# Kernel optimization log

Hardware: AMD Instinct MI355X
Metric: run time of the kernel (lower is better)

The kernel has to match this reference:

```python
import jax, jax.numpy as jnp
import numpy as np


def setup_inputs() -> dict:
    key = jax.random.key(0)
    k1, k2 = jax.random.split(key)
    B, Q, K, H = 8, 2048, 2048, 128
    out_state = jax.random.normal(k1, (B, Q, H), dtype=jnp.float32)
    history = jax.random.normal(k2, (B, K, H), dtype=jnp.float32)
    return {"out_state": out_state, "history": history}


def reference(out_state, history):
    # tanh pre-activation on queries
    q = jnp.tanh(out_state)                              # [B, Q, H]
    # unscaled QK^T scores
    scores = jnp.einsum("bqh,bkh->bqk", q, history)      # [B, Q, K]
    probs = jax.nn.softmax(scores, axis=2)               # softmax over keys
    attn = jnp.einsum("bqk,bkh->bqh", probs, history)    # [B, Q, H]
    return attn
```

## Files before the change

### kernel.cpp

```cpp
#include <hip/hip_runtime.h>
#include <math.h>


typedef _Float16 half8 __attribute__((ext_vector_type(8)));
typedef _Float16 half4 __attribute__((ext_vector_type(4)));
typedef float    f32x4 __attribute__((ext_vector_type(4)));

#define QQ 2048
#define KK 2048
#define HH 128
#define BM 64
#define BN 64
#define NTILES 32
#define KS_STR 136
#define VT_STR 72
#define PS_STR 72
#define L2E 1.44269504f
#define SPLITS_TARGET 3
#define WS_O_FLOATS   ((size_t)256 * BM * HH)
#define WS_ML_FLOATS  ((size_t)256 * BM)

union U32H { unsigned int u; _Float16 h[2]; };

__launch_bounds__(256, 3)
__global__ void attn_main(const float* __restrict__ out_state,
                          const float* __restrict__ history,
                          float* __restrict__ out,
                          float* __restrict__ ws,
                          int splits) {
    __shared__ _Float16 Ks[BN * KS_STR];
    __shared__ _Float16 Vt[HH * VT_STR];
    __shared__ _Float16 Ps[4][16 * PS_STR];

    const int tid  = threadIdx.x;
    const int wave = tid >> 6;
    const int lane = tid & 63;
    const int quad = lane >> 4;
    const int lc   = lane & 15;

    const int bid  = blockIdx.x;
    const int s    = bid >> 8;
    const int r256 = bid & 255;
    const int b    = r256 >> 5;
    const int qb   = r256 & 31;
    const int m0   = qb * BM;

    const int kt0 = (NTILES * s) / splits;
    const int kt1 = (NTILES * (s + 1)) / splits;

    half8 qf[4];
    {
        const int m = m0 + wave * 16 + lc;
        const float* qrow = out_state + ((size_t)b * QQ + m) * HH;
        #pragma unroll
        for (int s4 = 0; s4 < 4; ++s4) {
            const int h0 = 32 * s4 + quad * 8;
            const float4 a = *(const float4*)(qrow + h0);
            const float4 c = *(const float4*)(qrow + h0 + 4);
            qf[s4][0] = (_Float16)tanhf(a.x); qf[s4][1] = (_Float16)tanhf(a.y);
            qf[s4][2] = (_Float16)tanhf(a.z); qf[s4][3] = (_Float16)tanhf(a.w);
            qf[s4][4] = (_Float16)tanhf(c.x); qf[s4][5] = (_Float16)tanhf(c.y);
            qf[s4][6] = (_Float16)tanhf(c.z); qf[s4][7] = (_Float16)tanhf(c.w);
        }
    }

    const f32x4 zero4 = {0.f, 0.f, 0.f, 0.f};
    f32x4 O[8];
    #pragma unroll
    for (int i = 0; i < 8; ++i) O[i] = zero4;
    f32x4 Osum = zero4;
    float rmax = -3.0e38f;

    const int r0  = tid >> 5;
    const int c4  = (tid & 31) * 4;
    const int h0  = 2 * (tid & 63);
    const int n0t = (tid >> 6) * 16;

    const half8 ones = {(_Float16)1.f,(_Float16)1.f,(_Float16)1.f,(_Float16)1.f,
                        (_Float16)1.f,(_Float16)1.f,(_Float16)1.f,(_Float16)1.f};

    for (int kt = kt0; kt < kt1; ++kt) {
        const int n0 = kt * BN;

        float4 g[8];
        const float* hb = history + ((size_t)b * KK + n0) * HH;
        #pragma unroll
        for (int j = 0; j < 8; ++j)
            g[j] = *(const float4*)(hb + (size_t)(r0 + 8 * j) * HH + c4);

        __syncthreads();
        #pragma unroll
        for (int j = 0; j < 8; ++j) {
            half4 hv;
            hv[0] = (_Float16)g[j].x; hv[1] = (_Float16)g[j].y;
            hv[2] = (_Float16)g[j].z; hv[3] = (_Float16)g[j].w;
            *(half4*)&Ks[(r0 + 8 * j) * KS_STR + c4] = hv;
        }
        __syncthreads();
        {
            half8 ra0, ra1, rb0, rb1;
            #pragma unroll
            for (int i = 0; i < 8; ++i) {
                U32H t; t.u = *(const unsigned int*)&Ks[(n0t + i) * KS_STR + h0];
                ra0[i] = t.h[0]; rb0[i] = t.h[1];
            }
            #pragma unroll
            for (int i = 8; i < 16; ++i) {
                U32H t; t.u = *(const unsigned int*)&Ks[(n0t + i) * KS_STR + h0];
                ra1[i - 8] = t.h[0]; rb1[i - 8] = t.h[1];
            }
            *(half8*)&Vt[(h0    ) * VT_STR + n0t    ] = ra0;
            *(half8*)&Vt[(h0    ) * VT_STR + n0t + 8] = ra1;
            *(half8*)&Vt[(h0 + 1) * VT_STR + n0t    ] = rb0;
            *(half8*)&Vt[(h0 + 1) * VT_STR + n0t + 8] = rb1;
        }
        __syncthreads();

        f32x4 S[4];
        #pragma unroll
        for (int nt = 0; nt < 4; ++nt) {
            f32x4 acc = zero4;
            #pragma unroll
            for (int s4 = 0; s4 < 4; ++s4) {
                half8 kf = *(half8*)&Ks[(nt * 16 + lc) * KS_STR + 32 * s4 + quad * 8];
                acc = __builtin_amdgcn_mfma_f32_16x16x32_f16(kf, qf[s4], acc, 0, 0, 0);
            }
            S[nt] = acc;
        }

        float tmax = S[0][0];
        #pragma unroll
        for (int nt = 0; nt < 4; ++nt)
            #pragma unroll
            for (int r = 0; r < 4; ++r)
                tmax = fmaxf(tmax, S[nt][r]);
        tmax = fmaxf(tmax, __shfl_xor(tmax, 16, 64));
        tmax = fmaxf(tmax, __shfl_xor(tmax, 32, 64));

        const float nm = fmaxf(rmax, tmax);
        const float alpha = exp2f((rmax - nm) * L2E);
        rmax = nm;

        #pragma unroll
        for (int nt = 0; nt < 4; ++nt)
            #pragma unroll
            for (int r = 0; r < 4; ++r)
                S[nt][r] = exp2f((S[nt][r] - nm) * L2E);

        #pragma unroll
        for (int ct = 0; ct < 8; ++ct) O[ct] *= alpha;
        Osum *= alpha;

        #pragma unroll
        for (int nt = 0; nt < 4; ++nt) {
            half4 pv;
            pv[0] = (_Float16)S[nt][0]; pv[1] = (_Float16)S[nt][1];
            pv[2] = (_Float16)S[nt][2]; pv[3] = (_Float16)S[nt][3];
            *(half4*)&Ps[wave][lc * PS_STR + nt * 16 + quad * 4] = pv;
        }

        #pragma unroll
        for (int s2 = 0; s2 < 2; ++s2) {
            half8 pb = *(half8*)&Ps[wave][lc * PS_STR + s2 * 32 + quad * 8];
            Osum = __builtin_amdgcn_mfma_f32_16x16x32_f16(ones, pb, Osum, 0, 0, 0);
            #pragma unroll
            for (int ct = 0; ct < 8; ++ct) {
                half8 vf = *(half8*)&Vt[(ct * 16 + lc) * VT_STR + s2 * 32 + quad * 8];
                O[ct] = __builtin_amdgcn_mfma_f32_16x16x32_f16(vf, pb, O[ct], 0, 0, 0);
            }
        }
    }

    if (splits == 1) {
        const float inv = 1.0f / Osum[0];
        float* orow = out + ((size_t)b * QQ + m0 + wave * 16 + lc) * HH;
        #pragma unroll
        for (int ct = 0; ct < 8; ++ct) {
            f32x4 v = O[ct] * inv;
            *(f32x4*)&orow[ct * 16 + quad * 4] = v;
        }
    } else {
        float* po = ws + ((size_t)(s * 256 + r256)) * (BM * HH) + (wave * 16 + lc) * HH;
        #pragma unroll
        for (int ct = 0; ct < 8; ++ct)
            *(f32x4*)&po[ct * 16 + quad * 4] = O[ct];
        if (quad == 0) {
            const size_t mlBase = (size_t)splits * WS_O_FLOATS;
            const size_t idx = (size_t)(s * 256 + r256) * BM + wave * 16 + lc;
            ws[mlBase + idx] = rmax;
            ws[mlBase + (size_t)splits * WS_ML_FLOATS + idx] = Osum[0];
        }
    }
}

__global__ void attn_combine(const float* __restrict__ ws,
                             float* __restrict__ out,
                             int splits) {
    const int idx = blockIdx.x * 256 + threadIdx.x;
    const int h  = idx & 127;
    const int q  = (idx >> 7) & 2047;
    const int b  = idx >> 18;
    const int qb = q >> 6;
    const int qr = q & 63;
    const int blk = b * 32 + qb;

    const size_t mlBase = (size_t)splits * WS_O_FLOATS;
    const size_t lBase  = mlBase + (size_t)splits * WS_ML_FLOATS;

    float ms[4];
    float M = -3.0e38f;
    for (int s = 0; s < splits; ++s) {
        ms[s] = ws[mlBase + (size_t)(s * 256 + blk) * BM + qr];
        M = fmaxf(M, ms[s]);
    }
    float denom = 0.f, val = 0.f;
    for (int s = 0; s < splits; ++s) {
        const float w = exp2f((ms[s] - M) * L2E);
        denom += w * ws[lBase + (size_t)(s * 256 + blk) * BM + qr];
        val   += w * ws[(size_t)(s * 256 + blk) * (BM * HH) + qr * HH + h];
    }
    out[idx] = val / denom;
}

extern "C" void kernel_launch(void* const* d_in, const int* in_sizes, int n_in,
                              void* d_out, int out_size, void* d_ws, size_t ws_size,
                              hipStream_t stream) {
    const float* out_state = (const float*)d_in[0];
    const float* history   = (const float*)d_in[1];
    float* out = (float*)d_out;
    float* ws  = (float*)d_ws;

    const size_t needed = (size_t)SPLITS_TARGET * (WS_O_FLOATS + 2 * WS_ML_FLOATS) * 4;
    const int splits = (ws_size >= needed) ? SPLITS_TARGET : 1;

    attn_main<<<dim3(256 * splits), dim3(256), 0, stream>>>(out_state, history, out, ws, splits);
    if (splits > 1)
        attn_combine<<<dim3((8 * QQ * HH) / 256), dim3(256), 0, stream>>>(ws, out, splits);
}
```

Before: 119.8 us.

## Precompute fp16 swizzled K and V^T tiles, async-load into LDS with prefetch

A new prep kernel converts history to fp16 once, writing both a swizzled K layout and a pre-transposed V layout to workspace. The main kernel then streams these tiles straight into LDS with global_load_lds, prefetching the next K and V tile while the current one is computed. This removes the repeated per-block fp32 load, conversion and LDS transpose. It also skips the rescale when the running max does not change, raises wave priority around the MFMA sections, and stores split partials as normalized fp16 to cut combine traffic. In exchange it adds an extra launch, uses more workspace, and loses some precision in the partial outputs.

```diff
diff --git a/kernel.cpp b/kernel.cpp
--- a/kernel.cpp
+++ b/kernel.cpp
@@ -12,31 +12,113 @@
 #define BM 64
 #define BN 64
 #define NTILES 32
-#define KS_STR 136
-#define VT_STR 72
 #define PS_STR 72
 #define L2E 1.44269504f
 #define SPLITS_TARGET 3
-#define WS_O_FLOATS   ((size_t)256 * BM * HH)
-#define WS_ML_FLOATS  ((size_t)256 * BM)
+
+#define KS_STRP 136
+#define VT_STRP 72
+
+#define KH_HALVES     ((size_t)8 * KK * HH)
+#define PREP_BYTES    (KH_HALVES * 4)
+#define OSPLIT_BYTES  ((size_t)256 * BM * HH * 2)
+#define MLSPLIT_FLOATS ((size_t)256 * BM)
 
 union U32H { unsigned int u; _Float16 h[2]; };
+
+typedef __attribute__((address_space(1))) const void gvoid;
+typedef __attribute__((address_space(3))) void lvoid;
+
+#define WAITVM4 asm volatile("s_waitcnt vmcnt(4)" ::: "memory")
+#define WAITVM0 asm volatile("s_waitcnt vmcnt(0)" ::: "memory")
+static __device__ __forceinline__ void wgbar() {
+    asm volatile("" ::: "memory");
+    __builtin_amdgcn_s_barrier();
+    asm volatile("" ::: "memory");
+}
+
+__launch_bounds__(256)
+__global__ void attn_prep(const float* __restrict__ history,
+                          _Float16* __restrict__ wsh) {
+    __shared__ __align__(16) _Float16 Ks[BN * KS_STRP];
+    __shared__ __align__(16) _Float16 Vt[HH * VT_STRP];
+
+    const int tid = threadIdx.x;
+    const int bid = blockIdx.x;
+    const int b   = bid >> 5;
+    const int kt  = bid & 31;
+
+    const float* hb = history + ((size_t)b * KK + (size_t)kt * BN) * HH;
+    const int r0 = tid >> 5;
+    const int c4 = (tid & 31) * 4;
+    #pragma unroll
+    for (int j = 0; j < 8; ++j) {
+        const float4 g = *(const float4*)(hb + (size_t)(r0 + 8 * j) * HH + c4);
+        half4 hv;
+        hv[0] = (_Float16)g.x; hv[1] = (_Float16)g.y;
+        hv[2] = (_Float16)g.z; hv[3] = (_Float16)g.w;
+        *(half4*)&Ks[(r0 + 8 * j) * KS_STRP + c4] = hv;
+    }
+    __syncthreads();
+
+    {
+        const int h0  = 2 * (tid & 63);
+        const int n0t = (tid >> 6) * 16;
+        half8 ra0, ra1, rb0, rb1;
+        #pragma unroll
+        for (int i = 0; i < 8; ++i) {
+            U32H t; t.u = *(const unsigned int*)&Ks[(n0t + i) * KS_STRP + h0];
+            ra0[i] = t.h[0]; rb0[i] = t.h[1];
+        }
+        #pragma unroll
+        for (int i = 8; i < 16; ++i) {
+            U32H t; t.u = *(const unsigned int*)&Ks[(n0t + i) * KS_STRP + h0];
+            ra1[i - 8] = t.h[0]; rb1[i - 8] = t.h[1];
+        }
+        *(half8*)&Vt[(h0    ) * VT_STRP + n0t    ] = ra0;
+        *(half8*)&Vt[(h0    ) * VT_STRP + n0t + 8] = ra1;
+        *(half8*)&Vt[(h0 + 1) * VT_STRP + n0t    ] = rb0;
+        *(half8*)&Vt[(h0 + 1) * VT_STRP + n0t + 8] = rb1;
+    }
+
+    {
+        const int k  = tid >> 2;
+        const int c0 = (tid & 3) * 32;
+        const int sk = (k & 7) << 3;
+        _Float16* dst = wsh + ((size_t)b * KK + (size_t)kt * BN + k) * HH;
+        #pragma unroll
+        for (int g8 = 0; g8 < 4; ++g8)
+            *(half8*)&dst[(c0 + 8 * g8) ^ sk] = *(const half8*)&Ks[k * KS_STRP + c0 + 8 * g8];
+    }
+    __syncthreads();
+
+    {
+        const int h  = tid >> 1;
+        const int n0 = (tid & 1) * 32;
+        const int th = (h & 7) << 3;
+        _Float16* dst = wsh + KH_HALVES + (((size_t)b * NTILES + kt) * HH + h) * BN;
+        #pragma unroll
+        for (int g8 = 0; g8 < 4; ++g8)
+            *(half8*)&dst[(n0 + 8 * g8) ^ th] = *(const half8*)&Vt[h * VT_STRP + n0 + 8 * g8];
+    }
+}
 
 __launch_bounds__(256, 3)
 __global__ void attn_main(const float* __restrict__ out_state,
-                          const float* __restrict__ history,
+                          const _Float16* __restrict__ wsh,
                           float* __restrict__ out,
-                          float* __restrict__ ws,
+                          char* __restrict__ wsb,
                           int splits) {
-    __shared__ _Float16 Ks[BN * KS_STR];
-    __shared__ _Float16 Vt[HH * VT_STR];
-    __shared__ _Float16 Ps[4][16 * PS_STR];
+    __shared__ __align__(16) _Float16 Ks[BN * HH];
+    __shared__ __align__(16) _Float16 Vt[HH * BN];
+    __shared__ __align__(16) _Float16 Ps[4][16 * PS_STR];
 
     const int tid  = threadIdx.x;
     const int wave = tid >> 6;
     const int lane = tid & 63;
     const int quad = lane >> 4;
     const int lc   = lane & 15;
+    const int swz  = (lc & 7) << 3;
 
     const int bid  = blockIdx.x;
     const int s    = bid >> 8;
@@ -48,19 +130,47 @@
     const int kt0 = (NTILES * s) / splits;
     const int kt1 = (NTILES * (s + 1)) / splits;
 
+    const _Float16* khb = wsh + (size_t)b * KK * HH;
+    const _Float16* vtb = wsh + KH_HALVES + (size_t)b * NTILES * (HH * BN);
+
+    auto issueK = [&](int t) {
+        const char* gsrc = (const char*)(khb + (size_t)t * (BN * HH));
+        #pragma unroll
+        for (int c = 0; c < 4; ++c) {
+            const int off = (c * 4 + wave) * 1024 + lane * 16;
+            __builtin_amdgcn_global_load_lds((gvoid*)(gsrc + off),
+                                             (lvoid*)((char*)Ks + off), 16, 0, 0);
+        }
+    };
+    auto issueV = [&](int t) {
+        const char* gsrc = (const char*)(vtb + (size_t)t * (HH * BN));
+        #pragma unroll
+        for (int c = 0; c < 4; ++c) {
+            const int off = (c * 4 + wave) * 1024 + lane * 16;
+            __builtin_amdgcn_global_load_lds((gvoid*)(gsrc + off),
+                                             (lvoid*)((char*)Vt + off), 16, 0, 0);
+        }
+    };
+
+    issueK(kt0);
+    issueV(kt0);
+
     half8 qf[4];
     {
         const int m = m0 + wave * 16 + lc;
         const float* qrow = out_state + ((size_t)b * QQ + m) * HH;
+        float4 qa[8];
         #pragma unroll
         for (int s4 = 0; s4 < 4; ++s4) {
-            const int h0 = 32 * s4 + quad * 8;
-            const float4 a = *(const float4*)(qrow + h0);
-            const float4 c = *(const float4*)(qrow + h0 + 4);
-            qf[s4][0] = (_Float16)tanhf(a.x); qf[s4][1] = (_Float16)tanhf(a.y);
-            qf[s4][2] = (_Float16)tanhf(a.z); qf[s4][3] = (_Float16)tanhf(a.w);
-            qf[s4][4] = (_Float16)tanhf(c.x); qf[s4][5] = (_Float16)tanhf(c.y);
-            qf[s4][6] = (_Float16)tanhf(c.z); qf[s4][7] = (_Float16)tanhf(c.w);
+            qa[2 * s4]     = *(const float4*)(qrow + 32 * s4 + quad * 8);
+            qa[2 * s4 + 1] = *(const float4*)(qrow + 32 * s4 + quad * 8 + 4);
+        }
+        #pragma unroll
+        for (int s4 = 0; s4 < 4; ++s4) {
+            qf[s4][0] = (_Float16)tanhf(qa[2*s4].x);   qf[s4][1] = (_Float16)tanhf(qa[2*s4].y);
+            qf[s4][2] = (_Float16)tanhf(qa[2*s4].z);   qf[s4][3] = (_Float16)tanhf(qa[2*s4].w);
+            qf[s4][4] = (_Float16)tanhf(qa[2*s4+1].x); qf[s4][5] = (_Float16)tanhf(qa[2*s4+1].y);
+            qf[s4][6] = (_Float16)tanhf(qa[2*s4+1].z); qf[s4][7] = (_Float16)tanhf(qa[2*s4+1].w);
         }
     }
 
@@ -71,62 +181,32 @@
     f32x4 Osum = zero4;
     float rmax = -3.0e38f;
 
-    const int r0  = tid >> 5;
-    const int c4  = (tid & 31) * 4;
-    const int h0  = 2 * (tid & 63);
-    const int n0t = (tid >> 6) * 16;
-
     const half8 ones = {(_Float16)1.f,(_Float16)1.f,(_Float16)1.f,(_Float16)1.f,
                         (_Float16)1.f,(_Float16)1.f,(_Float16)1.f,(_Float16)1.f};
 
     for (int kt = kt0; kt < kt1; ++kt) {
-        const int n0 = kt * BN;
-
-        float4 g[8];
-        const float* hb = history + ((size_t)b * KK + n0) * HH;
-        #pragma unroll
-        for (int j = 0; j < 8; ++j)
-            g[j] = *(const float4*)(hb + (size_t)(r0 + 8 * j) * HH + c4);
-
-        __syncthreads();
-        #pragma unroll
-        for (int j = 0; j < 8; ++j) {
-            half4 hv;
-            hv[0] = (_Float16)g[j].x; hv[1] = (_Float16)g[j].y;
-            hv[2] = (_Float16)g[j].z; hv[3] = (_Float16)g[j].w;
-            *(half4*)&Ks[(r0 + 8 * j) * KS_STR + c4] = hv;
-        }
-        __syncthreads();
-        {
-            half8 ra0, ra1, rb0, rb1;
-            #pragma unroll
-            for (int i = 0; i < 8; ++i) {
-                U32H t; t.u = *(const unsigned int*)&Ks[(n0t + i) * KS_STR + h0];
-                ra0[i] = t.h[0]; rb0[i] = t.h[1];
-            }
-            #pragma unroll
-            for (int i = 8; i < 16; ++i) {
-                U32H t; t.u = *(const unsigned int*)&Ks[(n0t + i) * KS_STR + h0];
-                ra1[i - 8] = t.h[0]; rb1[i - 8] = t.h[1];
-            }
-            *(half8*)&Vt[(h0    ) * VT_STR + n0t    ] = ra0;
-            *(half8*)&Vt[(h0    ) * VT_STR + n0t + 8] = ra1;
-            *(half8*)&Vt[(h0 + 1) * VT_STR + n0t    ] = rb0;
-            *(half8*)&Vt[(h0 + 1) * VT_STR + n0t + 8] = rb1;
-        }
-        __syncthreads();
+        const bool more = (kt + 1 < kt1);
+
+        WAITVM4;
+        wgbar();
 
         f32x4 S[4];
+        __builtin_amdgcn_s_setprio(1);
         #pragma unroll
         for (int nt = 0; nt < 4; ++nt) {
             f32x4 acc = zero4;
             #pragma unroll
             for (int s4 = 0; s4 < 4; ++s4) {
-                half8 kf = *(half8*)&Ks[(nt * 16 + lc) * KS_STR + 32 * s4 + quad * 8];
+                const half8 kf = *(const half8*)
+                    &Ks[((nt * 16 + lc) << 7) + ((32 * s4 + (quad << 3)) ^ swz)];
                 acc = __builtin_amdgcn_mfma_f32_16x16x32_f16(kf, qf[s4], acc, 0, 0, 0);
             }
             S[nt] = acc;
         }
+        __builtin_amdgcn_s_setprio(0);
+
+        wgbar();
+        if (more) issueK(kt + 1);
 
         float tmax = S[0][0];
         #pragma unroll
@@ -137,19 +217,20 @@
         tmax = fmaxf(tmax, __shfl_xor(tmax, 16, 64));
         tmax = fmaxf(tmax, __shfl_xor(tmax, 32, 64));
 
-        const float nm = fmaxf(rmax, tmax);
-        const float alpha = exp2f((rmax - nm) * L2E);
-        rmax = nm;
+        if (!__all(tmax <= rmax)) {
+            const float nm    = fmaxf(rmax, tmax);
+            const float alpha = exp2f((rmax - nm) * L2E);
+            rmax = nm;
+            #pragma unroll
+            for (int ct = 0; ct < 8; ++ct) O[ct] *= alpha;
+            Osum *= alpha;
+        }
 
         #pragma unroll
         for (int nt = 0; nt < 4; ++nt)
             #pragma unroll
             for (int r = 0; r < 4; ++r)
-                S[nt][r] = exp2f((S[nt][r] - nm) * L2E);
-
-        #pragma unroll
-        for (int ct = 0; ct < 8; ++ct) O[ct] *= alpha;
-        Osum *= alpha;
+                S[nt][r] = exp2f((S[nt][r] - rmax) * L2E);
 
         #pragma unroll
         for (int nt = 0; nt < 4; ++nt) {
@@ -159,16 +240,25 @@
             *(half4*)&Ps[wave][lc * PS_STR + nt * 16 + quad * 4] = pv;
         }
 
+        if (more) { WAITVM4; } else { WAITVM0; }
+        wgbar();
+
+        __builtin_amdgcn_s_setprio(1);
         #pragma unroll
         for (int s2 = 0; s2 < 2; ++s2) {
-            half8 pb = *(half8*)&Ps[wave][lc * PS_STR + s2 * 32 + quad * 8];
+            const half8 pb = *(const half8*)&Ps[wave][lc * PS_STR + s2 * 32 + quad * 8];
             Osum = __builtin_amdgcn_mfma_f32_16x16x32_f16(ones, pb, Osum, 0, 0, 0);
             #pragma unroll
             for (int ct = 0; ct < 8; ++ct) {
-                half8 vf = *(half8*)&Vt[(ct * 16 + lc) * VT_STR + s2 * 32 + quad * 8];
+                const half8 vf = *(const half8*)
+                    &Vt[((ct * 16 + lc) << 6) + ((32 * s2 + (quad << 3)) ^ swz)];
                 O[ct] = __builtin_amdgcn_mfma_f32_16x16x32_f16(vf, pb, O[ct], 0, 0, 0);
             }
         }
+        __builtin_amdgcn_s_setprio(0);
+
+        wgbar();
+        if (more) issueV(kt + 1);
     }
 
     if (splits == 1) {
@@ -180,44 +270,53 @@
             *(f32x4*)&orow[ct * 16 + quad * 4] = v;
         }
     } else {
-        float* po = ws + ((size_t)(s * 256 + r256)) * (BM * HH) + (wave * 16 + lc) * HH;
-        #pragma unroll
-        for (int ct = 0; ct < 8; ++ct)
-            *(f32x4*)&po[ct * 16 + quad * 4] = O[ct];
+        const float inv = 1.0f / Osum[0];
+        _Float16* oh = (_Float16*)(wsb + PREP_BYTES)
+                     + ((size_t)(s * 256 + r256) * BM + wave * 16 + lc) * HH;
+        #pragma unroll
+        for (int ct = 0; ct < 8; ++ct) {
+            const f32x4 v = O[ct] * inv;
+            half4 hv;
+            hv[0] = (_Float16)v[0]; hv[1] = (_Float16)v[1];
+            hv[2] = (_Float16)v[2]; hv[3] = (_Float16)v[3];
+            *(half4*)&oh[ct * 16 + quad * 4] = hv;
+        }
         if (quad == 0) {
-            const size_t mlBase = (size_t)splits * WS_O_FLOATS;
+            float* wm = (float*)(wsb + PREP_BYTES + (size_t)splits * OSPLIT_BYTES);
             const size_t idx = (size_t)(s * 256 + r256) * BM + wave * 16 + lc;
-            ws[mlBase + idx] = rmax;
-            ws[mlBase + (size_t)splits * WS_ML_FLOATS + idx] = Osum[0];
-        }
-    }
-}
-
-__global__ void attn_combine(const float* __restrict__ ws,
+            wm[idx] = rmax;
+            wm[(size_t)splits * MLSPLIT_FLOATS + idx] = Osum[0];
+        }
+    }
+}
+
+__launch_bounds__(256)
+__global__ void attn_combine(const char* __restrict__ wsb,
                              float* __restrict__ out,
                              int splits) {
     const int idx = blockIdx.x * 256 + threadIdx.x;
-    const int h  = idx & 127;
-    const int q  = (idx >> 7) & 2047;
-    const int b  = idx >> 18;
-    const int qb = q >> 6;
-    const int qr = q & 63;
+    const int h   = idx & 127;
+    const int q   = (idx >> 7) & 2047;
+    const int b   = idx >> 18;
+    const int qb  = q >> 6;
+    const int qr  = q & 63;
     const int blk = b * 32 + qb;
 
-    const size_t mlBase = (size_t)splits * WS_O_FLOATS;
-    const size_t lBase  = mlBase + (size_t)splits * WS_ML_FLOATS;
-
-    float ms[4];
+    const _Float16* oh = (const _Float16*)(wsb + PREP_BYTES);
+    const float* wm = (const float*)(wsb + PREP_BYTES + (size_t)splits * OSPLIT_BYTES);
+    const float* wl = wm + (size_t)splits * MLSPLIT_FLOATS;
+
+    float ms[SPLITS_TARGET];
     float M = -3.0e38f;
     for (int s = 0; s < splits; ++s) {
-        ms[s] = ws[mlBase + (size_t)(s * 256 + blk) * BM + qr];
+        ms[s] = wm[(size_t)(s * 256 + blk) * BM + qr];
         M = fmaxf(M, ms[s]);
     }
     float denom = 0.f, val = 0.f;
     for (int s = 0; s < splits; ++s) {
-        const float w = exp2f((ms[s] - M) * L2E);
-        denom += w * ws[lBase + (size_t)(s * 256 + blk) * BM + qr];
-        val   += w * ws[(size_t)(s * 256 + blk) * (BM * HH) + qr * HH + h];
+        const float wgt = exp2f((ms[s] - M) * L2E) * wl[(size_t)(s * 256 + blk) * BM + qr];
+        denom += wgt;
+        val   += wgt * (float)oh[(size_t)(s * 256 + blk) * (BM * HH) + (size_t)qr * HH + h];
     }
     out[idx] = val / denom;
 }
@@ -228,12 +327,16 @@
     const float* out_state = (const float*)d_in[0];
     const float* history   = (const float*)d_in[1];
     float* out = (float*)d_out;
-    float* ws  = (float*)d_ws;
-
-    const size_t needed = (size_t)SPLITS_TARGET * (WS_O_FLOATS + 2 * WS_ML_FLOATS) * 4;
-    const int splits = (ws_size >= needed) ? SPLITS_TARGET : 1;
-
-    attn_main<<<dim3(256 * splits), dim3(256), 0, stream>>>(out_state, history, out, ws, splits);
+    char* wsb  = (char*)d_ws;
+
+    const size_t need3 = PREP_BYTES
+                       + (size_t)SPLITS_TARGET * OSPLIT_BYTES
+                       + (size_t)SPLITS_TARGET * 2 * MLSPLIT_FLOATS * 4;
+    const int splits = (ws_size >= need3) ? SPLITS_TARGET : 1;
+
+    attn_prep<<<dim3(256), dim3(256), 0, stream>>>(history, (_Float16*)wsb);
+    attn_main<<<dim3(256 * splits), dim3(256), 0, stream>>>(out_state, (const _Float16*)wsb,
+                                                            out, wsb, splits);
     if (splits > 1)
-        attn_combine<<<dim3((8 * QQ * HH) / 256), dim3(256), 0, stream>>>(ws, out, splits);
-}
+        attn_combine<<<dim3((8 * QQ * HH) / 256), dim3(256), 0, stream>>>(wsb, out, splits);
+}
```

After: 120.9 us. Within noise of the previous version (+0.9%).
